# Performance work log

Hardware: AMD Instinct MI355X
Metric: run time of the kernel (lower is better)

## Reference

```python
import jax, jax.numpy as jnp
import numpy as np
import math

B, S, D_IN, D_OUT, H = 2, 2048, 1024, 1024, 16
HD = D_OUT // H


def setup_inputs() -> dict:
    key = jax.random.key(0)
    ks = jax.random.split(key, 6)
    scale = 0.02
    return {
        "x": jax.random.normal(ks[0], (B, S, D_IN), dtype=jnp.float32),
        "Wq": jax.random.normal(ks[1], (D_IN, D_OUT), dtype=jnp.float32) * scale,
        "Wk": jax.random.normal(ks[2], (D_IN, D_OUT), dtype=jnp.float32) * scale,
        "Wv": jax.random.normal(ks[3], (D_IN, D_OUT), dtype=jnp.float32) * scale,
        "Wo": jax.random.normal(ks[4], (D_OUT, D_OUT), dtype=jnp.float32) * scale,
        "bo": jax.random.normal(ks[5], (D_OUT,), dtype=jnp.float32) * scale,
    }


def reference(x, Wq, Wk, Wv, Wo, bo):
    b, n, _ = x.shape
    # project and split heads -> [b, h, n, hd]
    q = (x @ Wq).reshape(b, n, H, HD).transpose(0, 2, 1, 3)
    k = (x @ Wk).reshape(b, n, H, HD).transpose(0, 2, 1, 3)
    v = (x @ Wv).reshape(b, n, H, HD).transpose(0, 2, 1, 3)
    # materialized [b, h, n, n] scores with causal mask (as in original)
    scores = jnp.einsum('bhqd,bhkd->bhqk', q, k)
    causal = jnp.tril(jnp.ones((n, n), dtype=bool))  # True = keep
    scores = jnp.where(causal, scores, -jnp.inf)
    attn = jax.nn.softmax(scores / math.sqrt(HD), axis=-1)
    ctx = jnp.einsum('bhqk,bhkd->bhqd', attn, v)
    ctx = ctx.transpose(0, 2, 1, 3).reshape(b, n, D_OUT)
    return ctx @ Wo + bo
```

## Files before the change

### kernel.cpp

```cpp
#include <hip/hip_runtime.h>
#include <hip/hip_bf16.h>
#include <math.h>

typedef __bf16 v8bf __attribute__((ext_vector_type(8)));
typedef __bf16 v4bf __attribute__((ext_vector_type(4)));
typedef short  v4s  __attribute__((ext_vector_type(4)));
typedef float  v4f  __attribute__((ext_vector_type(4)));
typedef unsigned short u16;

static_assert(sizeof(v8bf) == 16, "v8bf must be 16B");

__device__ __forceinline__ u16 f2bf(float f) {
  __hip_bfloat16 h = __float2bfloat16(f);
  return *reinterpret_cast<u16*>(&h);
}
__device__ __forceinline__ v4f mfma16(v8bf a, v8bf b, v4f c) {
  return __builtin_amdgcn_mfma_f32_16x16x32_bf16(a, b, c, 0, 0, 0);
}
__device__ __forceinline__ v4f mfma16k16(v4bf a, v4bf b, v4f c) {
#if __has_builtin(__builtin_amdgcn_mfma_f32_16x16x16_bf16)
  return __builtin_amdgcn_mfma_f32_16x16x16_bf16(a, b, c, 0, 0, 0);
#else
  union { v4bf f; v4s s; } ua, ub;
  ua.f = a; ub.f = b;
  return __builtin_amdgcn_mfma_f32_16x16x16bf16_1k(ua.s, ub.s, c, 0, 0, 0);
#endif
}
__device__ __forceinline__ void async16(const u16* g, u16* l) {
  __builtin_amdgcn_global_load_lds(
      (__attribute__((address_space(1))) void*)(void*)g,
      (__attribute__((address_space(3))) void*)l, 16, 0, 0);
}

__global__ void prep(const float* __restrict__ x, const float* __restrict__ Wq,
                     const float* __restrict__ Wk, const float* __restrict__ Wv,
                     const float* __restrict__ Wo, u16* __restrict__ Wt,
                     u16* __restrict__ xb) {
  int tx = threadIdx.x, ty = threadIdx.y;
  if (blockIdx.z == 4) {
    int bid = blockIdx.y * 32 + blockIdx.x;
    int i = (bid * 1024 + ty * 32 + tx) * 4;
    float4 v = *(const float4*)(x + i);
    ushort4 o;
    o.x = f2bf(v.x); o.y = f2bf(v.y); o.z = f2bf(v.z); o.w = f2bf(v.w);
    *(ushort4*)(xb + i) = o;
    return;
  }
  __shared__ float tile[32][33];
  const float* src = (blockIdx.z == 0) ? Wq : (blockIdx.z == 1) ? Wk : (blockIdx.z == 2) ? Wv : Wo;
  int k0 = blockIdx.x * 32, n0 = blockIdx.y * 32;
  tile[ty][tx] = src[(size_t)(k0 + ty) * 1024 + n0 + tx];
  __syncthreads();
  Wt[(size_t)(blockIdx.z * 1024 + n0 + ty) * 1024 + k0 + tx] = f2bf(tile[tx][ty]);
}

__device__ __forceinline__ void gemm_core(const u16* __restrict__ A, const u16* __restrict__ Bt,
                                          u16* sA, u16* sB, v4f acc[4][4], int bm, int bn) {
  const int t = threadIdx.x;
  const int w = t >> 6, l = t & 63;
  const int quad = l >> 4, low = l & 15;
  const int wm = (w & 1) * 64, wn = (w >> 1) * 64;
  const int rowA = bm * 128 + w * 32 + (l >> 2);
  const int rowB = bn * 128 + w * 32 + (l >> 2);
  const int col8 = (l & 3) * 8;
  u16* la = sA + w * 1024;
  u16* lb = sB + w * 1024;

  for (int kb = 0; kb < 1024; kb += 32) {
    async16(A + (size_t)rowA * 1024 + kb + col8, la);
    async16(A + (size_t)(rowA + 16) * 1024 + kb + col8, la + 512);
    async16(Bt + (size_t)rowB * 1024 + kb + col8, lb);
    async16(Bt + (size_t)(rowB + 16) * 1024 + kb + col8, lb + 512);
    __syncthreads();
    v8bf af[4], bfr[4];
#pragma unroll
    for (int i = 0; i < 4; i++)
      af[i] = *(const v8bf*)(sA + (wm + i * 16 + low) * 32 + quad * 8);
#pragma unroll
    for (int j = 0; j < 4; j++)
      bfr[j] = *(const v8bf*)(sB + (wn + j * 16 + low) * 32 + quad * 8);
#pragma unroll
    for (int i = 0; i < 4; i++)
#pragma unroll
      for (int j = 0; j < 4; j++)
        acc[i][j] = mfma16(af[i], bfr[j], acc[i][j]);
    __syncthreads();
  }
}

__global__ __launch_bounds__(256) void gemm_qkv(const u16* __restrict__ xb,
                                                const u16* __restrict__ Wt,
                                                u16* __restrict__ Qb,
                                                u16* __restrict__ Kb,
                                                u16* __restrict__ Vt) {
  __shared__ __align__(16) u16 sA[128 * 32];
  __shared__ __align__(16) u16 sB[128 * 32];
  v4f acc[4][4] = {};
  const int bm = blockIdx.x, bn = blockIdx.y;
  gemm_core(xb, Wt, sA, sB, acc, bm, bn);
  const int t = threadIdx.x, w = t >> 6, l = t & 63, quad = l >> 4, low = l & 15;
  const int wm = (w & 1) * 64, wn = (w >> 1) * 64;
  const int zone = (bn * 128) >> 10;
  const float qsc = (zone == 0) ? 0.18033688011112042f : 1.0f;
#pragma unroll
  for (int i = 0; i < 4; i++) {
    int m0 = bm * 128 + wm + i * 16 + quad * 4;
#pragma unroll
    for (int j = 0; j < 4; j++) {
      int nn = (bn * 128 + wn + j * 16 + low) & 1023;
      if (zone == 0) {
#pragma unroll
        for (int r = 0; r < 4; r++)
          Qb[(size_t)(m0 + r) * 1024 + nn] = f2bf(acc[i][j][r] * qsc);
      } else if (zone == 1) {
#pragma unroll
        for (int r = 0; r < 4; r++)
          Kb[(size_t)(m0 + r) * 1024 + nn] = f2bf(acc[i][j][r]);
      } else {
        int bb = m0 >> 11, s = m0 & 2047;
#pragma unroll
        for (int r = 0; r < 4; r++)
          Vt[(size_t)(bb * 1024 + nn) * 2048 + s + r] = f2bf(acc[i][j][r]);
      }
    }
  }
}

__global__ __launch_bounds__(256) void gemm_out(const u16* __restrict__ ctx,
                                                const u16* __restrict__ Wt,
                                                const float* __restrict__ bo,
                                                float* __restrict__ out) {
  __shared__ __align__(16) u16 sA[128 * 32];
  __shared__ __align__(16) u16 sB[64 * 32];
  const u16* Bt = Wt + (size_t)3072 * 1024;
  v4f acc[4][2] = {};
  const int bm = blockIdx.x, bn = blockIdx.y;
  const int t = threadIdx.x, w = t >> 6, l = t & 63, quad = l >> 4, low = l & 15;
  const int wm = (w & 1) * 64, wn = (w >> 1) * 32;
  const int rowA = bm * 128 + w * 32 + (l >> 2);
  const int rowB = bn * 64 + w * 16 + (l >> 2);
  const int col8 = (l & 3) * 8;
  u16* la = sA + w * 1024;
  u16* lb = sB + w * 512;

  for (int kb = 0; kb < 1024; kb += 32) {
    async16(ctx + (size_t)rowA * 1024 + kb + col8, la);
    async16(ctx + (size_t)(rowA + 16) * 1024 + kb + col8, la + 512);
    async16(Bt + (size_t)rowB * 1024 + kb + col8, lb);
    __syncthreads();
    v8bf af[4], bfr[2];
#pragma unroll
    for (int i = 0; i < 4; i++)
      af[i] = *(const v8bf*)(sA + (wm + i * 16 + low) * 32 + quad * 8);
#pragma unroll
    for (int j = 0; j < 2; j++)
      bfr[j] = *(const v8bf*)(sB + (wn + j * 16 + low) * 32 + quad * 8);
#pragma unroll
    for (int i = 0; i < 4; i++)
#pragma unroll
      for (int j = 0; j < 2; j++)
        acc[i][j] = mfma16(af[i], bfr[j], acc[i][j]);
    __syncthreads();
  }
#pragma unroll
  for (int i = 0; i < 4; i++) {
    int m0 = bm * 128 + wm + i * 16 + quad * 4;
#pragma unroll
    for (int j = 0; j < 2; j++) {
      int n = bn * 64 + wn + j * 16 + low;
      float bias = bo[n];
#pragma unroll
      for (int r = 0; r < 4; r++)
        out[(size_t)(m0 + r) * 1024 + n] = acc[i][j][r] + bias;
    }
  }
}

__global__ __launch_bounds__(256) void attn(const u16* __restrict__ Qb,
                                            const u16* __restrict__ Kb,
                                            const u16* __restrict__ Vt,
                                            u16* __restrict__ ctx) {
  __shared__ __align__(16) u16 sK[4][4096];
  __shared__ __align__(16) u16 sV[4][4096];
  const int t = threadIdx.x, w = t >> 6, l = t & 63, quad = l >> 4, low = l & 15;

  const int bid = blockIdx.x;
  const int xcd = bid & 7, slot = bid >> 3;
  const int pair = xcd * 4 + (slot & 3);
  const int tp = slot >> 2;
  const int b = pair >> 4, h = pair & 15;

  const u16* kbase = Kb + (size_t)(b * 2048) * 1024 + h * 64;
  const u16* vbase = Vt + (size_t)(b * 1024 + h * 64) * 2048;

  const int srow = l >> 3;
  const int cg = (l & 7) ^ srow;

  auto STAGE = [&](int tt, int bi) {
    const int kb = tt * 64;
    const u16* kg = kbase + (size_t)(kb + w * 8 + srow) * 1024 + cg * 8;
    async16(kg, &sK[bi][w * 512]);
    async16(kg + (size_t)32 * 1024, &sK[bi][2048 + w * 512]);
    const u16* vg = vbase + (size_t)(w * 8 + srow) * 2048 + kb + cg * 8;
    async16(vg, &sV[bi][w * 512]);
    async16(vg + (size_t)32 * 2048, &sV[bi][2048 + w * 512]);
  };

  for (int ph = 0; ph < 2; ++ph) {
    const int tile = ph ? tp : 31 - tp;
    const int nkt = tile + 1;
    const int qw = tile * 64 + w * 16;

    if (ph) {
      asm volatile("s_waitcnt lgkmcnt(0)" ::: "memory");
      __builtin_amdgcn_s_barrier();
    }

    const u16* qrow_p = Qb + (size_t)(b * 2048 + qw + low) * 1024 + h * 64;
    v8bf qa0 = *(const v8bf*)(qrow_p + quad * 8);
    v8bf qa1 = *(const v8bf*)(qrow_p + 32 + quad * 8);
    asm volatile("" ::: "memory");

    float li = 0.f;
    v4f o[4] = {};

    STAGE(0, 0);
    if (nkt > 1) STAGE(1, 1);

    for (int it = 0; it < nkt; ++it) {
      const int bi = it & 3;
      if (it + 2 < nkt) STAGE(it + 2, (it + 2) & 3);
      asm volatile("s_waitcnt lgkmcnt(0)" ::: "memory");
      const int c = nkt - 1 - it;
      if (c >= 2)      asm volatile("s_waitcnt vmcnt(8)" ::: "memory");
      else if (c == 1) asm volatile("s_waitcnt vmcnt(4)" ::: "memory");
      else             asm volatile("s_waitcnt vmcnt(0)" ::: "memory");
      __builtin_amdgcn_s_barrier();

      const int kb = it * 64;
      v4f s[4] = {};
      __builtin_amdgcn_s_setprio(1);
#pragma unroll
      for (int cf = 0; cf < 4; cf++) {
        const int key = cf * 16 + low;
        v8bf kf0 = *(const v8bf*)(&sK[bi][key * 64 + ((quad ^ (key & 7)) * 8)]);
        v8bf kf1 = *(const v8bf*)(&sK[bi][key * 64 + (((4 + quad) ^ (key & 7)) * 8)]);
        s[cf] = mfma16(kf0, qa0, s[cf]);
        s[cf] = mfma16(kf1, qa1, s[cf]);
      }
      __builtin_amdgcn_s_setprio(0);

      const bool dm = (it == nkt - 1);
      const int qr = qw + low;
      v4bf pf[4];
#pragma unroll
      for (int cf = 0; cf < 4; cf++)
#pragma unroll
        for (int r = 0; r < 4; r++) {
          float e = __builtin_amdgcn_exp2f(s[cf][r]);
          if (dm && (kb + cf * 16 + quad * 4 + r > qr)) e = 0.f;
          li += e;
          pf[cf][r] = (__bf16)e;
        }

      __builtin_amdgcn_s_setprio(1);
#pragma unroll
      for (int df = 0; df < 4; df++) {
        const int d = df * 16 + low;
#pragma unroll
        for (int cf = 0; cf < 4; cf++) {
          const int c2 = cf * 2 + (quad >> 1);
          const v4bf vf = *(const v4bf*)(&sV[bi][d * 64 + ((c2 ^ (d & 7)) * 8) + (quad & 1) * 4]);
          o[df] = mfma16k16(pf[cf], vf, o[df]);
        }
      }
      __builtin_amdgcn_s_setprio(0);
    }

    li += __shfl_xor(li, 16);
    li += __shfl_xor(li, 32);

#pragma unroll
    for (int r = 0; r < 4; r++) {
      float lir = __shfl(li, quad * 4 + r);
      float inv = 1.f / lir;
      int row = b * 2048 + qw + quad * 4 + r;
#pragma unroll
      for (int df = 0; df < 4; df++)
        ctx[(size_t)row * 1024 + h * 64 + df * 16 + low] = f2bf(o[df][r] * inv);
    }
  }
}

extern "C" void kernel_launch(void* const* d_in, const int* in_sizes, int n_in,
                              void* d_out, int out_size, void* d_ws, size_t ws_size,
                              hipStream_t stream) {
  const float* x  = (const float*)d_in[0];
  const float* Wq = (const float*)d_in[1];
  const float* Wk = (const float*)d_in[2];
  const float* Wv = (const float*)d_in[3];
  const float* Wo = (const float*)d_in[4];
  const float* bo = (const float*)d_in[5];
  float* out = (float*)d_out;

  char* ws = (char*)d_ws;
  u16* xb  = (u16*)(ws);
  u16* Wt  = (u16*)(ws + 8ull * 1024 * 1024);
  u16* Qb  = (u16*)(ws + 16ull * 1024 * 1024);
  u16* Kb  = (u16*)(ws + 24ull * 1024 * 1024);
  u16* Vt  = (u16*)(ws + 32ull * 1024 * 1024);
  u16* ctx = (u16*)(ws + 40ull * 1024 * 1024);

  prep<<<dim3(32, 32, 5), dim3(32, 32, 1), 0, stream>>>(x, Wq, Wk, Wv, Wo, Wt, xb);
  gemm_qkv<<<dim3(32, 24, 1), dim3(256, 1, 1), 0, stream>>>(xb, Wt, Qb, Kb, Vt);
  attn<<<dim3(512, 1, 1), dim3(256, 1, 1), 0, stream>>>(Qb, Kb, Vt, ctx);
  gemm_out<<<dim3(32, 16, 1), dim3(256, 1, 1), 0, stream>>>(ctx, Wt, bo, out);
}
```

Before: 175.5 us.

## Split attention work into one query tile per block with 32-key KV tiles

The attention kernel no longer processes a paired long and short causal query tile in each block. It launches 1024 blocks, each handling a single 64-row query tile, and orders the tiles so long and short ones interleave across XCDs. The KV staging tile shrinks from 64 to 32 keys, with adjusted swizzles, which halves LDS usage and should allow more resident blocks. The cost is twice as many loop iterations and barriers per key range, masking on the last two tiles, and Q reloads per block, with load balance now left to the hardware scheduler.

```diff
diff --git a/kernel.cpp b/kernel.cpp
--- a/kernel.cpp
+++ b/kernel.cpp
@@ -180,115 +180,105 @@
                                             const u16* __restrict__ Kb,
                                             const u16* __restrict__ Vt,
                                             u16* __restrict__ ctx) {
-  __shared__ __align__(16) u16 sK[4][4096];
-  __shared__ __align__(16) u16 sV[4][4096];
+  __shared__ __align__(16) u16 sK[4][2048];
+  __shared__ __align__(16) u16 sV[4][2048];
   const int t = threadIdx.x, w = t >> 6, l = t & 63, quad = l >> 4, low = l & 15;
 
   const int bid = blockIdx.x;
-  const int xcd = bid & 7, slot = bid >> 3;
-  const int pair = xcd * 4 + (slot & 3);
-  const int tp = slot >> 2;
+  const int xcd = bid & 7, idx = bid >> 3;
+  const int c = idx & 31, j = idx >> 5;
+  const int pair = xcd * 4 + (c & 3);
+  const int u = c >> 2;
+  const int tile = (j == 0) ? (31 - u) : (j == 1) ? u : (j == 2) ? (23 - u) : (8 + u);
   const int b = pair >> 4, h = pair & 15;
+
+  const int nkt = 2 * tile + 2;
+  const int qw = tile * 64 + w * 16;
 
   const u16* kbase = Kb + (size_t)(b * 2048) * 1024 + h * 64;
   const u16* vbase = Vt + (size_t)(b * 1024 + h * 64) * 2048;
 
-  const int srow = l >> 3;
-  const int cg = (l & 7) ^ srow;
+  const int ksrow = l >> 3, kcg = (l & 7) ^ ksrow;
+  const int vsrow = l >> 2, vcg = (l & 3) ^ (vsrow & 3);
 
   auto STAGE = [&](int tt, int bi) {
-    const int kb = tt * 64;
-    const u16* kg = kbase + (size_t)(kb + w * 8 + srow) * 1024 + cg * 8;
-    async16(kg, &sK[bi][w * 512]);
-    async16(kg + (size_t)32 * 1024, &sK[bi][2048 + w * 512]);
-    const u16* vg = vbase + (size_t)(w * 8 + srow) * 2048 + kb + cg * 8;
-    async16(vg, &sV[bi][w * 512]);
-    async16(vg + (size_t)32 * 2048, &sV[bi][2048 + w * 512]);
+    const int kb = tt * 32;
+    async16(kbase + (size_t)(kb + w * 8 + ksrow) * 1024 + kcg * 8, &sK[bi][w * 512]);
+    async16(vbase + (size_t)(w * 16 + vsrow) * 2048 + kb + vcg * 8, &sV[bi][w * 512]);
   };
 
-  for (int ph = 0; ph < 2; ++ph) {
-    const int tile = ph ? tp : 31 - tp;
-    const int nkt = tile + 1;
-    const int qw = tile * 64 + w * 16;
-
-    if (ph) {
-      asm volatile("s_waitcnt lgkmcnt(0)" ::: "memory");
-      __builtin_amdgcn_s_barrier();
+  const u16* qrow_p = Qb + (size_t)(b * 2048 + qw + low) * 1024 + h * 64;
+  v8bf qa0 = *(const v8bf*)(qrow_p + quad * 8);
+  v8bf qa1 = *(const v8bf*)(qrow_p + 32 + quad * 8);
+  asm volatile("" ::: "memory");
+
+  float li = 0.f;
+  v4f o[4] = {};
+
+  STAGE(0, 0);
+  STAGE(1, 1);
+
+  for (int it = 0; it < nkt; ++it) {
+    const int bi = it & 3;
+    if (it + 2 < nkt) STAGE(it + 2, (it + 2) & 3);
+    asm volatile("s_waitcnt lgkmcnt(0)" ::: "memory");
+    const int cc = nkt - 1 - it;
+    if (cc >= 2)      asm volatile("s_waitcnt vmcnt(4)" ::: "memory");
+    else if (cc == 1) asm volatile("s_waitcnt vmcnt(2)" ::: "memory");
+    else              asm volatile("s_waitcnt vmcnt(0)" ::: "memory");
+    __builtin_amdgcn_s_barrier();
+
+    const int kb = it * 32;
+    v4f s[2] = {};
+    __builtin_amdgcn_s_setprio(1);
+#pragma unroll
+    for (int cf = 0; cf < 2; cf++) {
+      const int key = cf * 16 + low;
+      v8bf kf0 = *(const v8bf*)(&sK[bi][key * 64 + ((quad ^ (key & 7)) * 8)]);
+      v8bf kf1 = *(const v8bf*)(&sK[bi][key * 64 + (((4 + quad) ^ (key & 7)) * 8)]);
+      s[cf] = mfma16(kf0, qa0, s[cf]);
+      s[cf] = mfma16(kf1, qa1, s[cf]);
     }
-
-    const u16* qrow_p = Qb + (size_t)(b * 2048 + qw + low) * 1024 + h * 64;
-    v8bf qa0 = *(const v8bf*)(qrow_p + quad * 8);
-    v8bf qa1 = *(const v8bf*)(qrow_p + 32 + quad * 8);
-    asm volatile("" ::: "memory");
-
-    float li = 0.f;
-    v4f o[4] = {};
-
-    STAGE(0, 0);
-    if (nkt > 1) STAGE(1, 1);
-
-    for (int it = 0; it < nkt; ++it) {
-      const int bi = it & 3;
-      if (it + 2 < nkt) STAGE(it + 2, (it + 2) & 3);
-      asm volatile("s_waitcnt lgkmcnt(0)" ::: "memory");
-      const int c = nkt - 1 - it;
-      if (c >= 2)      asm volatile("s_waitcnt vmcnt(8)" ::: "memory");
-      else if (c == 1) asm volatile("s_waitcnt vmcnt(4)" ::: "memory");
-      else             asm volatile("s_waitcnt vmcnt(0)" ::: "memory");
-      __builtin_amdgcn_s_barrier();
-
-      const int kb = it * 64;
-      v4f s[4] = {};
-      __builtin_amdgcn_s_setprio(1);
-#pragma unroll
-      for (int cf = 0; cf < 4; cf++) {
-        const int key = cf * 16 + low;
-        v8bf kf0 = *(const v8bf*)(&sK[bi][key * 64 + ((quad ^ (key & 7)) * 8)]);
-        v8bf kf1 = *(const v8bf*)(&sK[bi][key * 64 + (((4 + quad) ^ (key & 7)) * 8)]);
-        s[cf] = mfma16(kf0, qa0, s[cf]);
-        s[cf] = mfma16(kf1, qa1, s[cf]);
+    __builtin_amdgcn_s_setprio(0);
+
+    const bool dm = (it >= nkt - 2);
+    const int qr = qw + low;
+    v4bf pf[2];
+#pragma unroll
+    for (int cf = 0; cf < 2; cf++)
+#pragma unroll
+      for (int r = 0; r < 4; r++) {
+        float e = __builtin_amdgcn_exp2f(s[cf][r]);
+        if (dm && (kb + cf * 16 + quad * 4 + r > qr)) e = 0.f;
+        li += e;
+        pf[cf][r] = (__bf16)e;
       }
-      __builtin_amdgcn_s_setprio(0);
-
-      const bool dm = (it == nkt - 1);
-      const int qr = qw + low;
-      v4bf pf[4];
-#pragma unroll
-      for (int cf = 0; cf < 4; cf++)
-#pragma unroll
-        for (int r = 0; r < 4; r++) {
-          float e = __builtin_amdgcn_exp2f(s[cf][r]);
-          if (dm && (kb + cf * 16 + quad * 4 + r > qr)) e = 0.f;
-          li += e;
-          pf[cf][r] = (__bf16)e;
-        }
-
-      __builtin_amdgcn_s_setprio(1);
-#pragma unroll
-      for (int df = 0; df < 4; df++) {
-        const int d = df * 16 + low;
-#pragma unroll
-        for (int cf = 0; cf < 4; cf++) {
-          const int c2 = cf * 2 + (quad >> 1);
-          const v4bf vf = *(const v4bf*)(&sV[bi][d * 64 + ((c2 ^ (d & 7)) * 8) + (quad & 1) * 4]);
-          o[df] = mfma16k16(pf[cf], vf, o[df]);
-        }
+
+    __builtin_amdgcn_s_setprio(1);
+#pragma unroll
+    for (int df = 0; df < 4; df++) {
+      const int d = df * 16 + low;
+#pragma unroll
+      for (int cf = 0; cf < 2; cf++) {
+        const int c2 = cf * 2 + (quad >> 1);
+        const v4bf vf = *(const v4bf*)(&sV[bi][d * 32 + ((c2 ^ (d & 3)) * 8) + (quad & 1) * 4]);
+        o[df] = mfma16k16(pf[cf], vf, o[df]);
       }
-      __builtin_amdgcn_s_setprio(0);
     }
-
-    li += __shfl_xor(li, 16);
-    li += __shfl_xor(li, 32);
-
-#pragma unroll
-    for (int r = 0; r < 4; r++) {
-      float lir = __shfl(li, quad * 4 + r);
-      float inv = 1.f / lir;
-      int row = b * 2048 + qw + quad * 4 + r;
-#pragma unroll
-      for (int df = 0; df < 4; df++)
-        ctx[(size_t)row * 1024 + h * 64 + df * 16 + low] = f2bf(o[df][r] * inv);
-    }
+    __builtin_amdgcn_s_setprio(0);
+  }
+
+  li += __shfl_xor(li, 16);
+  li += __shfl_xor(li, 32);
+
+#pragma unroll
+  for (int r = 0; r < 4; r++) {
+    float lir = __shfl(li, quad * 4 + r);
+    float inv = 1.f / lir;
+    int row = b * 2048 + qw + quad * 4 + r;
+#pragma unroll
+    for (int df = 0; df < 4; df++)
+      ctx[(size_t)row * 1024 + h * 64 + df * 16 + low] = f2bf(o[df][r] * inv);
   }
 }
 
@@ -313,6 +303,6 @@
 
   prep<<<dim3(32, 32, 5), dim3(32, 32, 1), 0, stream>>>(x, Wq, Wk, Wv, Wo, Wt, xb);
   gemm_qkv<<<dim3(32, 24, 1), dim3(256, 1, 1), 0, stream>>>(xb, Wt, Qb, Kb, Vt);
-  attn<<<dim3(512, 1, 1), dim3(256, 1, 1), 0, stream>>>(Qb, Kb, Vt, ctx);
+  attn<<<dim3(1024, 1, 1), dim3(256, 1, 1), 0, stream>>>(Qb, Kb, Vt, ctx);
   gemm_out<<<dim3(32, 16, 1), dim3(256, 1, 1), 0, stream>>>(ctx, Wt, bo, out);
 }
```

Result: slower. 193.7 us (+10.3%).

## Double GEMM K-tile to 64 and XOR-swizzle LDS layout to avoid bank conflicts

Applied to the files above, without the earlier changes.

Both projection GEMMs now stage a 64-wide K slice per iteration instead of 32, which halves the number of barrier pairs and loop iterations. Global-to-LDS async copies write rows with an XOR swizzle on the 16-byte column group, and fragment reads apply the same swizzle so that 16 lanes reading different rows hit different banks. LDS use per block doubles, which may lower occupancy, and the loop is still single-buffered.

```diff
diff --git a/kernel.cpp b/kernel.cpp
--- a/kernel.cpp
+++ b/kernel.cpp
@@ -60,30 +60,38 @@
   const int w = t >> 6, l = t & 63;
   const int quad = l >> 4, low = l & 15;
   const int wm = (w & 1) * 64, wn = (w >> 1) * 64;
-  const int rowA = bm * 128 + w * 32 + (l >> 2);
-  const int rowB = bn * 128 + w * 32 + (l >> 2);
-  const int col8 = (l & 3) * 8;
-  u16* la = sA + w * 1024;
-  u16* lb = sB + w * 1024;
-
-  for (int kb = 0; kb < 1024; kb += 32) {
-    async16(A + (size_t)rowA * 1024 + kb + col8, la);
-    async16(A + (size_t)(rowA + 16) * 1024 + kb + col8, la + 512);
-    async16(Bt + (size_t)rowB * 1024 + kb + col8, lb);
-    async16(Bt + (size_t)(rowB + 16) * 1024 + kb + col8, lb + 512);
+  const int srow = l >> 3;
+  const int cg = (l & 7) ^ srow;
+  const int rowAg = bm * 128 + w * 32 + srow;
+  const int rowBg = bn * 128 + w * 32 + srow;
+
+  for (int kb = 0; kb < 1024; kb += 64) {
+#pragma unroll
+    for (int g = 0; g < 4; g++) {
+      async16(A  + (size_t)(rowAg + g * 8) * 1024 + kb + cg * 8, sA + w * 2048 + g * 512);
+      async16(Bt + (size_t)(rowBg + g * 8) * 1024 + kb + cg * 8, sB + w * 2048 + g * 512);
+    }
     __syncthreads();
-    v8bf af[4], bfr[4];
-#pragma unroll
-    for (int i = 0; i < 4; i++)
-      af[i] = *(const v8bf*)(sA + (wm + i * 16 + low) * 32 + quad * 8);
-#pragma unroll
-    for (int j = 0; j < 4; j++)
-      bfr[j] = *(const v8bf*)(sB + (wn + j * 16 + low) * 32 + quad * 8);
-#pragma unroll
-    for (int i = 0; i < 4; i++)
-#pragma unroll
-      for (int j = 0; j < 4; j++)
-        acc[i][j] = mfma16(af[i], bfr[j], acc[i][j]);
+    v8bf af[2][4], bf[2][4];
+#pragma unroll
+    for (int i = 0; i < 4; i++) {
+      const int r = wm + i * 16 + low, sw = r & 7;
+      af[0][i] = *(const v8bf*)(sA + r * 64 + ((quad ^ sw) * 8));
+      af[1][i] = *(const v8bf*)(sA + r * 64 + (((4 + quad) ^ sw) * 8));
+    }
+#pragma unroll
+    for (int j = 0; j < 4; j++) {
+      const int r = wn + j * 16 + low, sw = r & 7;
+      bf[0][j] = *(const v8bf*)(sB + r * 64 + ((quad ^ sw) * 8));
+      bf[1][j] = *(const v8bf*)(sB + r * 64 + (((4 + quad) ^ sw) * 8));
+    }
+#pragma unroll
+    for (int kk = 0; kk < 2; kk++)
+#pragma unroll
+      for (int i = 0; i < 4; i++)
+#pragma unroll
+        for (int j = 0; j < 4; j++)
+          acc[i][j] = mfma16(af[kk][i], bf[kk][j], acc[i][j]);
     __syncthreads();
   }
 }
@@ -93,8 +101,8 @@
                                                 u16* __restrict__ Qb,
                                                 u16* __restrict__ Kb,
                                                 u16* __restrict__ Vt) {
-  __shared__ __align__(16) u16 sA[128 * 32];
-  __shared__ __align__(16) u16 sB[128 * 32];
+  __shared__ __align__(16) u16 sA[128 * 64];
+  __shared__ __align__(16) u16 sB[128 * 64];
   v4f acc[4][4] = {};
   const int bm = blockIdx.x, bn = blockIdx.y;
   gemm_core(xb, Wt, sA, sB, acc, bm, bn);
@@ -130,36 +138,46 @@
                                                 const u16* __restrict__ Wt,
                                                 const float* __restrict__ bo,
                                                 float* __restrict__ out) {
-  __shared__ __align__(16) u16 sA[128 * 32];
-  __shared__ __align__(16) u16 sB[64 * 32];
+  __shared__ __align__(16) u16 sA[128 * 64];
+  __shared__ __align__(16) u16 sB[64 * 64];
   const u16* Bt = Wt + (size_t)3072 * 1024;
   v4f acc[4][2] = {};
   const int bm = blockIdx.x, bn = blockIdx.y;
   const int t = threadIdx.x, w = t >> 6, l = t & 63, quad = l >> 4, low = l & 15;
   const int wm = (w & 1) * 64, wn = (w >> 1) * 32;
-  const int rowA = bm * 128 + w * 32 + (l >> 2);
-  const int rowB = bn * 64 + w * 16 + (l >> 2);
-  const int col8 = (l & 3) * 8;
-  u16* la = sA + w * 1024;
-  u16* lb = sB + w * 512;
-
-  for (int kb = 0; kb < 1024; kb += 32) {
-    async16(ctx + (size_t)rowA * 1024 + kb + col8, la);
-    async16(ctx + (size_t)(rowA + 16) * 1024 + kb + col8, la + 512);
-    async16(Bt + (size_t)rowB * 1024 + kb + col8, lb);
+  const int srow = l >> 3;
+  const int cg = (l & 7) ^ srow;
+  const int rowAg = bm * 128 + w * 32 + srow;
+  const int rowBg = bn * 64 + w * 16 + srow;
+
+  for (int kb = 0; kb < 1024; kb += 64) {
+#pragma unroll
+    for (int g = 0; g < 4; g++)
+      async16(ctx + (size_t)(rowAg + g * 8) * 1024 + kb + cg * 8, sA + w * 2048 + g * 512);
+#pragma unroll
+    for (int g = 0; g < 2; g++)
+      async16(Bt + (size_t)(rowBg + g * 8) * 1024 + kb + cg * 8, sB + w * 1024 + g * 512);
     __syncthreads();
-    v8bf af[4], bfr[2];
-#pragma unroll
-    for (int i = 0; i < 4; i++)
-      af[i] = *(const v8bf*)(sA + (wm + i * 16 + low) * 32 + quad * 8);
-#pragma unroll
-    for (int j = 0; j < 2; j++)
-      bfr[j] = *(const v8bf*)(sB + (wn + j * 16 + low) * 32 + quad * 8);
-#pragma unroll
-    for (int i = 0; i < 4; i++)
-#pragma unroll
-      for (int j = 0; j < 2; j++)
-        acc[i][j] = mfma16(af[i], bfr[j], acc[i][j]);
+    v8bf af[2][4], bf[2][2];
+#pragma unroll
+    for (int i = 0; i < 4; i++) {
+      const int r = wm + i * 16 + low, sw = r & 7;
+      af[0][i] = *(const v8bf*)(sA + r * 64 + ((quad ^ sw) * 8));
+      af[1][i] = *(const v8bf*)(sA + r * 64 + (((4 + quad) ^ sw) * 8));
+    }
+#pragma unroll
+    for (int j = 0; j < 2; j++) {
+      const int r = wn + j * 16 + low, sw = r & 7;
+      bf[0][j] = *(const v8bf*)(sB + r * 64 + ((quad ^ sw) * 8));
+      bf[1][j] = *(const v8bf*)(sB + r * 64 + (((4 + quad) ^ sw) * 8));
+    }
+#pragma unroll
+    for (int kk = 0; kk < 2; kk++)
+#pragma unroll
+      for (int i = 0; i < 4; i++)
+#pragma unroll
+        for (int j = 0; j < 2; j++)
+          acc[i][j] = mfma16(af[kk][i], bf[kk][j], acc[i][j]);
     __syncthreads();
   }
 #pragma unroll
```

Result: slower. 181.3 us (+3.3%).

## Rewrite QKV GEMM with 256x256 tiles, double-buffered swizzled LDS pipeline

Applied to the files above, without the earlier changes.

Moves the QKV projection GEMM from 128x128 tiles with single-buffered 32-wide K steps to 256x256 tiles with 512 threads and 64-wide K steps. Shared memory is double-buffered, and the next tile's async loads are interleaved with the MFMA phases using vmcnt waits and raised wave priority. The LDS layout is XOR-swizzled to avoid bank conflicts. This uses 128KB of dynamic LDS and gives 192 blocks, which lowers occupancy and leaves partial wave coverage across the CUs in exchange for more data reuse and overlap of loads with compute.

```diff
diff --git a/kernel.cpp b/kernel.cpp
--- a/kernel.cpp
+++ b/kernel.cpp
@@ -54,60 +54,103 @@
   Wt[(size_t)(blockIdx.z * 1024 + n0 + ty) * 1024 + k0 + tx] = f2bf(tile[tx][ty]);
 }
 
-__device__ __forceinline__ void gemm_core(const u16* __restrict__ A, const u16* __restrict__ Bt,
-                                          u16* sA, u16* sB, v4f acc[4][4], int bm, int bn) {
-  const int t = threadIdx.x;
-  const int w = t >> 6, l = t & 63;
-  const int quad = l >> 4, low = l & 15;
-  const int wm = (w & 1) * 64, wn = (w >> 1) * 64;
-  const int rowA = bm * 128 + w * 32 + (l >> 2);
-  const int rowB = bn * 128 + w * 32 + (l >> 2);
-  const int col8 = (l & 3) * 8;
-  u16* la = sA + w * 1024;
-  u16* lb = sB + w * 1024;
-
-  for (int kb = 0; kb < 1024; kb += 32) {
-    async16(A + (size_t)rowA * 1024 + kb + col8, la);
-    async16(A + (size_t)(rowA + 16) * 1024 + kb + col8, la + 512);
-    async16(Bt + (size_t)rowB * 1024 + kb + col8, lb);
-    async16(Bt + (size_t)(rowB + 16) * 1024 + kb + col8, lb + 512);
-    __syncthreads();
-    v8bf af[4], bfr[4];
-#pragma unroll
-    for (int i = 0; i < 4; i++)
-      af[i] = *(const v8bf*)(sA + (wm + i * 16 + low) * 32 + quad * 8);
-#pragma unroll
-    for (int j = 0; j < 4; j++)
-      bfr[j] = *(const v8bf*)(sB + (wn + j * 16 + low) * 32 + quad * 8);
-#pragma unroll
-    for (int i = 0; i < 4; i++)
-#pragma unroll
-      for (int j = 0; j < 4; j++)
-        acc[i][j] = mfma16(af[i], bfr[j], acc[i][j]);
-    __syncthreads();
-  }
-}
-
-__global__ __launch_bounds__(256) void gemm_qkv(const u16* __restrict__ xb,
+__global__ __launch_bounds__(512) void gemm_qkv(const u16* __restrict__ xb,
                                                 const u16* __restrict__ Wt,
                                                 u16* __restrict__ Qb,
                                                 u16* __restrict__ Kb,
                                                 u16* __restrict__ Vt) {
-  __shared__ __align__(16) u16 sA[128 * 32];
-  __shared__ __align__(16) u16 sB[128 * 32];
-  v4f acc[4][4] = {};
+  extern __shared__ __align__(16) u16 lds[];
+  u16* sA = lds;
+  u16* sB = lds + 32768;
+
+  const int t = threadIdx.x;
+  const int w = t >> 6, l = t & 63;
+  const int quad = l >> 4, low = l & 15;
+  const int wm = (w & 1) * 128, wn = (w >> 1) * 64;
   const int bm = blockIdx.x, bn = blockIdx.y;
-  gemm_core(xb, Wt, sA, sB, acc, bm, bn);
-  const int t = threadIdx.x, w = t >> 6, l = t & 63, quad = l >> 4, low = l & 15;
-  const int wm = (w & 1) * 64, wn = (w >> 1) * 64;
-  const int zone = (bn * 128) >> 10;
+
+  const int srow = l >> 3;
+  const int cg = (l & 7) ^ srow;
+
+  auto SA_ = [&](int R0, int kb, u16* dst) {
+    async16(xb + (size_t)(bm * 256 + R0 + w * 8 + srow) * 1024 + kb + cg * 8,
+            dst + (R0 + w * 8) * 64);
+  };
+  auto SB_ = [&](int R0, int kb, u16* dst) {
+    async16(Wt + (size_t)(bn * 256 + R0 + w * 8 + srow) * 1024 + kb + cg * 8,
+            dst + (R0 + w * 8) * 64);
+  };
+
+  v4f acc[8][4] = {};
+
+  SB_(0, 0, sB); SB_(64, 0, sB); SB_(128, 0, sB); SB_(192, 0, sB);
+  SA_(0, 0, sA); SA_(128, 0, sA); SA_(64, 0, sA); SA_(192, 0, sA);
+
+#pragma unroll 2
+  for (int kt = 0; kt < 16; ++kt) {
+    const int p = kt & 1;
+    const u16* pa = sA + p * 16384;
+    const u16* pb = sB + p * 16384;
+    u16* nA = sA + (p ^ 1) * 16384;
+    u16* nB = sB + (p ^ 1) * 16384;
+    const int nkb = (kt + 1) * 64;
+    const bool more = (kt < 15);
+
+    asm volatile("s_waitcnt lgkmcnt(0)" ::: "memory");
+    asm volatile("s_waitcnt vmcnt(2)" ::: "memory");
+    __builtin_amdgcn_s_barrier();
+
+    v8bf bf[2][4];
+#pragma unroll
+    for (int j = 0; j < 4; j++) {
+      const int rb = wn + j * 16 + low, sw = rb & 7;
+      bf[0][j] = *(const v8bf*)(pb + rb * 64 + ((quad ^ sw) * 8));
+      bf[1][j] = *(const v8bf*)(pb + rb * 64 + (((4 + quad) ^ sw) * 8));
+    }
+#pragma unroll
+    for (int ph = 0; ph < 4; ++ph) {
+      if (ph == 2) {
+        if (more) asm volatile("s_waitcnt vmcnt(4)" ::: "memory");
+        else      asm volatile("s_waitcnt vmcnt(0)" ::: "memory");
+        __builtin_amdgcn_s_barrier();
+      }
+      v8bf a0k0, a0k1, a1k0, a1k1;
+      {
+        const int ra = wm + (2 * ph) * 16 + low, sw = ra & 7;
+        a0k0 = *(const v8bf*)(pa + ra * 64 + ((quad ^ sw) * 8));
+        a0k1 = *(const v8bf*)(pa + ra * 64 + (((4 + quad) ^ sw) * 8));
+      }
+      {
+        const int ra = wm + (2 * ph + 1) * 16 + low, sw = ra & 7;
+        a1k0 = *(const v8bf*)(pa + ra * 64 + ((quad ^ sw) * 8));
+        a1k1 = *(const v8bf*)(pa + ra * 64 + (((4 + quad) ^ sw) * 8));
+      }
+      if (more) {
+        if (ph == 0)      { SB_(0, nkb, nB);   SB_(64, nkb, nB); }
+        else if (ph == 1) { SB_(128, nkb, nB); SB_(192, nkb, nB); }
+        else if (ph == 2) { SA_(0, nkb, nA);   SA_(128, nkb, nA); }
+        else              { SA_(64, nkb, nA);  SA_(192, nkb, nA); }
+      }
+      __builtin_amdgcn_s_setprio(1);
+#pragma unroll
+      for (int j = 0; j < 4; j++) {
+        acc[2 * ph][j]     = mfma16(a0k0, bf[0][j], acc[2 * ph][j]);
+        acc[2 * ph][j]     = mfma16(a0k1, bf[1][j], acc[2 * ph][j]);
+        acc[2 * ph + 1][j] = mfma16(a1k0, bf[0][j], acc[2 * ph + 1][j]);
+        acc[2 * ph + 1][j] = mfma16(a1k1, bf[1][j], acc[2 * ph + 1][j]);
+      }
+      __builtin_amdgcn_s_setprio(0);
+    }
+  }
+
+  const int zone = bn >> 2;
   const float qsc = (zone == 0) ? 0.18033688011112042f : 1.0f;
 #pragma unroll
-  for (int i = 0; i < 4; i++) {
-    int m0 = bm * 128 + wm + i * 16 + quad * 4;
+  for (int i = 0; i < 8; i++) {
+    int m0 = bm * 256 + wm + i * 16 + quad * 4;
 #pragma unroll
     for (int j = 0; j < 4; j++) {
-      int nn = (bn * 128 + wn + j * 16 + low) & 1023;
+      int nn = (bn * 256 + wn + j * 16 + low) & 1023;
       if (zone == 0) {
 #pragma unroll
         for (int r = 0; r < 4; r++)
@@ -311,8 +354,15 @@
   u16* Vt  = (u16*)(ws + 32ull * 1024 * 1024);
   u16* ctx = (u16*)(ws + 40ull * 1024 * 1024);
 
+  static bool cfg = false;
+  if (!cfg) {
+    hipFuncSetAttribute((const void*)gemm_qkv,
+                        hipFuncAttributeMaxDynamicSharedMemorySize, 131072);
+    cfg = true;
+  }
+
   prep<<<dim3(32, 32, 5), dim3(32, 32, 1), 0, stream>>>(x, Wq, Wk, Wv, Wo, Wt, xb);
-  gemm_qkv<<<dim3(32, 24, 1), dim3(256, 1, 1), 0, stream>>>(xb, Wt, Qb, Kb, Vt);
+  gemm_qkv<<<dim3(16, 12, 1), dim3(512, 1, 1), 131072, stream>>>(xb, Wt, Qb, Kb, Vt);
   attn<<<dim3(512, 1, 1), dim3(256, 1, 1), 0, stream>>>(Qb, Kb, Vt, ctx);
   gemm_out<<<dim3(32, 16, 1), dim3(256, 1, 1), 0, stream>>>(ctx, Wt, bo, out);
 }
```

New measurement: 175.7 us. No clear change (+0.1%).
